# Optimization experiments

Hardware: AMD Instinct MI355X
Metric: run time of the kernel (lower is better)

The kernel has to match this reference:

```python
import jax, jax.numpy as jnp
import numpy as np

B, C, H_IMG, W_IMG = 16, 384, 56, 56
NUM_HEADS = 6
HEAD_DIM = C // NUM_HEADS
BN_EPS = 1e-5


def _bn(x, gamma, beta, mean, var):
    # x: [b, ch, n] or [b, ch, h, w]; per-channel affine normalization (eval-mode BatchNorm)
    shape = (1, -1) + (1,) * (x.ndim - 2)
    scale = (gamma / jnp.sqrt(var + BN_EPS)).reshape(shape)
    shift = (beta - mean * gamma / jnp.sqrt(var + BN_EPS)).reshape(shape)
    return x * scale + shift


def setup_inputs() -> dict:
    key = jax.random.key(0)
    ks = jax.random.split(key, 12)
    c2 = 2 * C
    return {
        "x": jax.random.normal(ks[0], (B, C, H_IMG, W_IMG), jnp.float32),
        "qk_w": jax.random.normal(ks[1], (c2, C // 2), jnp.float32) * 0.05,
        "qk_gamma": jax.random.uniform(ks[2], (c2,), jnp.float32, 0.5, 1.5),
        "qk_beta": jax.random.normal(ks[3], (c2,), jnp.float32) * 0.1,
        "qk_mean": jax.random.normal(ks[4], (c2,), jnp.float32) * 0.1,
        "qk_var": jax.random.uniform(ks[5], (c2,), jnp.float32, 0.5, 1.5),
        "pe_w": jax.random.normal(ks[6], (C, 1, 3, 3), jnp.float32) * 0.1,
        "pe_gamma": jax.random.uniform(ks[7], (C,), jnp.float32, 0.5, 1.5),
        "pe_beta": jax.random.normal(ks[8], (C,), jnp.float32) * 0.1,
        "pe_mean": jax.random.normal(ks[9], (C,), jnp.float32) * 0.1,
        "pe_var": jax.random.uniform(ks[10], (C,), jnp.float32, 0.5, 1.5),
    }


def reference(x, qk_w, qk_gamma, qk_beta, qk_mean, qk_var,
              pe_w, pe_gamma, pe_beta, pe_mean, pe_var):
    b, c, h, w = x.shape
    n = h * w
    s = n ** (-0.5)
    nh, hd = NUM_HEADS, HEAD_DIM

    # grouped (groups=2) 1x1 conv: out channels [0:c] from input [0:c/2], [c:2c] from [c/2:c]
    xg = x.reshape(b, 2, c // 2, n)                       # [b, 2, c/2, n]
    wg = qk_w.reshape(2, c, c // 2)                       # [group, out_per_group, in_per_group]
    qk = jnp.einsum('bgin,goi->bgon', xg, wg).reshape(b, 2 * c, n)
    qk = _bn(qk, qk_gamma, qk_beta, qk_mean, qk_var)
    qk = jax.nn.elu(qk) + 1.0

    qk = qk.reshape(b, 2, nh, hd, n)
    q, k = qk[:, 0], qk[:, 1]                             # [b, H, d, n]
    v = x.reshape(b, nh, hd, n)                           # [b, H, d, n]

    # kv = (k*s) @ (v^T * s): [b, H, d, d]
    kv = jnp.einsum('bhdn,bhen->bhde', k * s, v * s)
    # numerator: q^T @ kv -> [b, H, n, d]
    num = jnp.einsum('bhdn,bhde->bhne', q, kv)
    # denominator: q^T @ mean_n(k) -> [b, H, n]
    den = jnp.einsum('bhdn,bhd->bhn', q, k.mean(axis=-1)) + 1e-6
    attn = (num / den[..., None]).transpose(0, 1, 3, 2).reshape(b, c, h, w)

    # depthwise 3x3 conv positional encoding on v (= x) + BN
    pe = jax.lax.conv_general_dilated(
        x, pe_w, window_strides=(1, 1), padding=((1, 1), (1, 1)),
        feature_group_count=c, dimension_numbers=('NCHW', 'OIHW', 'NCHW'))
    pe = _bn(pe, pe_gamma, pe_beta, pe_mean, pe_var)

    return attn + pe
```

## Files before the change

kernel.cpp:

```cpp
#include <hip/hip_runtime.h>
#include <math.h>

#define N_SP 3136
#define BN_EPS 1e-5f

typedef __attribute__((ext_vector_type(8))) short short8;
typedef __attribute__((ext_vector_type(4))) float f32x4;

#define K_SZ    (16*384*N_SP)
#define KVP_OFF (K_SZ)
#define KVP_SZ  (16*6*7*64*80)
#define KVT_OFF (KVP_OFF + KVP_SZ)
#define KVT_FSZ (2*96*80*64/2)
#define WH_OFF  (KVT_OFF + KVT_FSZ)
#define WSPLIT_N (2*384*192)
#define WF_G    (384*192)
#define PWS_OFF (WH_OFF + WSPLIT_N)
#define PSH_OFF (PWS_OFF + 384*9)
#define QSC_OFF (PSH_OFF + 384)
#define QSH_OFF (QSC_OFF + 384)

#define FSWZ(n) ((((n) >> 1) ^ ((n) >> 2)) & 7)

__device__ __forceinline__ void bsplit(float f, ushort& h, ushort& l) {
    uint u = __float_as_uint(f);
    uint hr = (u + 0x7FFFu + ((u >> 16) & 1u)) >> 16;
    h = (ushort)hr;
    float fh = __uint_as_float(hr << 16);
    float fl = f - fh;
    uint v = __float_as_uint(fl);
    l = (ushort)((v + 0x7FFFu + ((v >> 16) & 1u)) >> 16);
}

__global__ __launch_bounds__(256) void p0_prep(
    const float* __restrict__ qk_w, const float* __restrict__ pe_w,
    const float* __restrict__ qk_gamma, const float* __restrict__ qk_beta,
    const float* __restrict__ qk_mean, const float* __restrict__ qk_var,
    const float* __restrict__ pgamma, const float* __restrict__ pbeta,
    const float* __restrict__ pmean, const float* __restrict__ pvar,
    ushort* __restrict__ wfh, ushort* __restrict__ wfl,
    float* __restrict__ pwsc, float* __restrict__ psh,
    float* __restrict__ qsc, float* __restrict__ qsh)
{
    int idx = blockIdx.x * 256 + threadIdx.x;
    if (idx < WSPLIT_N) {
        int g = (idx >= WF_G) ? 1 : 0;
        int rem = idx - g * WF_G;
        int row = rem / 192, k = rem % 192;
        ushort h, l;
        bsplit(qk_w[idx], h, l);
        int dst = g * WF_G + ((row >> 4) * 24 + (k >> 3)) * 128 + (row & 15) * 8 + (k & 7);
        wfh[dst] = h;
        wfl[dst] = l;
    }
    if (idx < 384) {
        float sc = pgamma[idx] / sqrtf(pvar[idx] + BN_EPS);
        psh[idx] = pbeta[idx] - pmean[idx] * sc;
        #pragma unroll
        for (int q = 0; q < 9; ++q) pwsc[idx * 9 + q] = pe_w[idx * 9 + q] * sc;
        float qs = qk_gamma[idx] / sqrtf(qk_var[idx] + BN_EPS);
        qsc[idx] = qs;
        qsh[idx] = qk_beta[idx] - qk_mean[idx] * qs;
    }
}

__global__ __launch_bounds__(256, 4) void k1_k_mfma(
    const float* __restrict__ x, const ushort* __restrict__ wfh, const ushort* __restrict__ wfl,
    const float* __restrict__ gamma, const float* __restrict__ beta,
    const float* __restrict__ mean, const float* __restrict__ var,
    uint* __restrict__ kq)
{
    __shared__ __align__(16) ushort Bh[4096];
    __shared__ __align__(16) ushort Bl[4096];
    __shared__ float scs[192], shs[192];

    const int bx = blockIdx.x;
    const int by = blockIdx.y;
    const int b = blockIdx.z;
    const int t = threadIdx.x;
    const int lane = t & 63, wv = t >> 6;
    const int lg = lane >> 4, l15 = lane & 15;

    f32x4 acc[3][4];
    #pragma unroll
    for (int mf = 0; mf < 3; ++mf)
        #pragma unroll
        for (int nf = 0; nf < 4; ++nf)
            acc[mf][nf] = (f32x4){0.f, 0.f, 0.f, 0.f};

    const float* xg = x + (size_t)(b * 384 + 192) * N_SP + bx * 64;
    const ushort* wfbh = wfh + WF_G;
    const ushort* wfbl = wfl + WF_G;

    for (int i = t; i < 192; i += 256) {
        int ch = 384 + by * 192 + i;
        float sc = gamma[ch] / sqrtf(var[ch] + BN_EPS);
        scs[i] = sc;
        shs[i] = beta[ch] - mean[ch] * sc;
    }

    for (int kt = 0; kt < 3; ++kt) {
        #pragma unroll
        for (int li = 0; li < 2; ++li) {
            int idx = li * 256 + t;
            int kp = idx >> 4;
            int nq = idx & 15;
            int k0 = kp * 2;
            const float* px = xg + (size_t)(kt * 64 + k0) * N_SP + nq * 4;
            float4 v0 = *(const float4*)px;
            float4 v1 = *(const float4*)(px + N_SP);
            ushort h0[4], l0[4], h1[4], l1[4];
            float a0[4] = {v0.x, v0.y, v0.z, v0.w};
            float a1[4] = {v1.x, v1.y, v1.z, v1.w};
            #pragma unroll
            for (int i2 = 0; i2 < 4; ++i2) { bsplit(a0[i2], h0[i2], l0[i2]); bsplit(a1[i2], h1[i2], l1[i2]); }
            int kb = k0 >> 3, ks = kp & 3;
            #pragma unroll
            for (int i2 = 0; i2 < 4; ++i2) {
                int n = nq * 4 + i2;
                int chunk = n * 8 + (kb ^ FSWZ(n));
                ((uint*)Bh)[chunk * 4 + ks] = (uint)h0[i2] | ((uint)h1[i2] << 16);
                ((uint*)Bl)[chunk * 4 + ks] = (uint)l0[i2] | ((uint)l1[i2] << 16);
            }
        }
        __syncthreads();
        #pragma unroll
        for (int s = 0; s < 2; ++s) {
            int kbq = s * 4 + lg;
            int kglob = kt * 8 + kbq;
            short8 bh[4], bl[4];
            #pragma unroll
            for (int nf = 0; nf < 4; ++nf) {
                int n = nf * 16 + l15;
                int chunk = n * 8 + (kbq ^ FSWZ(n));
                bh[nf] = *(const short8*)&Bh[chunk * 8];
                bl[nf] = *(const short8*)&Bl[chunk * 8];
            }
            #pragma unroll
            for (int mf = 0; mf < 3; ++mf) {
                int rb = by * 12 + wv * 3 + mf;
                int off = (rb * 24 + kglob) * 128 + l15 * 8;
                short8 ah = *(const short8*)&wfbh[off];
                short8 al = *(const short8*)&wfbl[off];
                #pragma unroll
                for (int nf = 0; nf < 4; ++nf) {
                    acc[mf][nf] = __builtin_amdgcn_mfma_f32_16x16x32_bf16(ah, bh[nf], acc[mf][nf], 0, 0, 0);
                    acc[mf][nf] = __builtin_amdgcn_mfma_f32_16x16x32_bf16(ah, bl[nf], acc[mf][nf], 0, 0, 0);
                    acc[mf][nf] = __builtin_amdgcn_mfma_f32_16x16x32_bf16(al, bh[nf], acc[mf][nf], 0, 0, 0);
                }
            }
        }
        __syncthreads();
    }

    size_t obase = ((size_t)b * 384 + by * 192) * N_SP + bx * 64;
    #pragma unroll
    for (int mf = 0; mf < 3; ++mf)
        #pragma unroll
        for (int nf = 0; nf < 4; ++nf) {
            #pragma unroll
            for (int r = 0; r < 4; ++r) {
                int lrow = wv * 48 + mf * 16 + lg * 4 + r;
                float v = acc[mf][nf][r] * scs[lrow] + shs[lrow];
                v = v > 0.f ? v + 1.f : __expf(v);
                ushort hh, ll;
                bsplit(v, hh, ll);
                kq[obase + (size_t)lrow * N_SP + nf * 16 + l15] = (uint)hh | ((uint)ll << 16);
            }
        }
}

__global__ __launch_bounds__(256) void k2_kv_mfma(
    const float* __restrict__ x, const uint* __restrict__ kq,
    float* __restrict__ kv_part)
{
    __shared__ __align__(16) ushort Kh[4096], Kl[4096];
    __shared__ __align__(16) ushort Vh[5120], Vl[5120];

    const int chunk = blockIdx.x;
    const int h = blockIdx.y, b = blockIdx.z;
    const int t = threadIdx.x;
    const int lane = t & 63, wv = t >> 6;
    const int lg = lane >> 4, l15 = lane & 15;

    const uint* kp  = kq + (size_t)(b*384 + h*64) * N_SP;
    const float* vp = x  + (size_t)(b*384 + h*64) * N_SP;

    #pragma unroll
    for (int li = 0; li < 4; ++li) {
        int idx = li * 256 + t;
        int row = 64 + (idx >> 6), col = idx & 63;
        int off = (row * 8 + ((col >> 3) ^ (row & 7))) * 8 + (col & 7);
        Vh[off] = (row == 64) ? (ushort)0x3F80 : (ushort)0;
        Vl[off] = 0;
    }

    f32x4 acc[5];
    #pragma unroll
    for (int nf = 0; nf < 5; ++nf) acc[nf] = (f32x4){0.f, 0.f, 0.f, 0.f};

    for (int sub = 0; sub < 7; ++sub) {
        int n0 = chunk * 448 + sub * 64;
        #pragma unroll
        for (int li = 0; li < 4; ++li) {
            int idx = li * 256 + t;
            int row = idx >> 4, sc = idx & 15;
            int off = (row * 8 + ((sc >> 1) ^ (row & 7))) * 8 + (sc & 1) * 4;
            uint4 kf = *(const uint4*)&kp[(size_t)row * N_SP + n0 + sc * 4];
            ((uint*)&Kh[off])[0] = (kf.x & 0xFFFFu) | (kf.y << 16);
            ((uint*)&Kh[off])[1] = (kf.z & 0xFFFFu) | (kf.w << 16);
            ((uint*)&Kl[off])[0] = (kf.x >> 16) | (kf.y & 0xFFFF0000u);
            ((uint*)&Kl[off])[1] = (kf.z >> 16) | (kf.w & 0xFFFF0000u);
            float4 vf = *(const float4*)&vp[(size_t)row * N_SP + n0 + sc * 4];
            ushort h0,h1,h2,h3,l0,l1,l2,l3;
            bsplit(vf.x,h0,l0); bsplit(vf.y,h1,l1); bsplit(vf.z,h2,l2); bsplit(vf.w,h3,l3);
            ((uint*)&Vh[off])[0] = (uint)h0 | ((uint)h1 << 16);
            ((uint*)&Vh[off])[1] = (uint)h2 | ((uint)h3 << 16);
            ((uint*)&Vl[off])[0] = (uint)l0 | ((uint)l1 << 16);
            ((uint*)&Vl[off])[1] = (uint)l2 | ((uint)l3 << 16);
        }
        __syncthreads();
        #pragma unroll
        for (int s = 0; s < 2; ++s) {
            int arow = wv * 16 + l15;
            int akb = (s * 4 + lg) ^ (arow & 7);
            short8 ah = *(const short8*)&Kh[(arow * 8 + akb) * 8];
            short8 al = *(const short8*)&Kl[(arow * 8 + akb) * 8];
            #pragma unroll
            for (int nf = 0; nf < 5; ++nf) {
                int brow = nf * 16 + l15;
                int bkb = (s * 4 + lg) ^ (brow & 7);
                short8 bh = *(const short8*)&Vh[(brow * 8 + bkb) * 8];
                short8 bl = *(const short8*)&Vl[(brow * 8 + bkb) * 8];
                acc[nf] = __builtin_amdgcn_mfma_f32_16x16x32_bf16(ah, bh, acc[nf], 0, 0, 0);
                acc[nf] = __builtin_amdgcn_mfma_f32_16x16x32_bf16(ah, bl, acc[nf], 0, 0, 0);
                acc[nf] = __builtin_amdgcn_mfma_f32_16x16x32_bf16(al, bh, acc[nf], 0, 0, 0);
            }
        }
        __syncthreads();
    }

    size_t base = (size_t)((b*6 + h)*7 + chunk) * 64 * 80;
    #pragma unroll
    for (int nf = 0; nf < 5; ++nf)
        #pragma unroll
        for (int r = 0; r < 4; ++r) {
            int d = wv * 16 + lg * 4 + r;
            kv_part[base + (size_t)d * 80 + nf * 16 + l15] = acc[nf][r];
        }
}

__global__ __launch_bounds__(256) void k2b_reduce(
    const float* __restrict__ kv_part,
    ushort* __restrict__ kvt_h, ushort* __restrict__ kvt_l)
{
    const int bh = blockIdx.x;
    const int t = threadIdx.x;
    const float inv_n = 1.0f / (float)N_SP;
    const float* base = kv_part + (size_t)bh * 7 * 5120;
    ushort* oh = kvt_h + (size_t)bh * 5120;
    ushort* ol = kvt_l + (size_t)bh * 5120;
    float s[20];
    #pragma unroll
    for (int j = 0; j < 20; ++j) s[j] = 0.f;
    for (int c = 0; c < 7; ++c) {
        #pragma unroll
        for (int j = 0; j < 20; ++j) s[j] += base[c * 5120 + j * 256 + t];
    }
    #pragma unroll
    for (int j = 0; j < 20; ++j) {
        int i = j * 256 + t;
        int d = i / 80, e = i % 80;
        ushort h, l;
        bsplit(s[j] * inv_n, h, l);
        oh[e * 64 + d] = h;
        ol[e * 64 + d] = l;
    }
}

#define ATT_STRIDE 68
__global__ __launch_bounds__(256, 4) void k3_attn_pe(
    const float* __restrict__ x,
    const ushort* __restrict__ wfh, const ushort* __restrict__ wfl,
    const float* __restrict__ qsc, const float* __restrict__ qsh,
    const ushort* __restrict__ kvt_h, const ushort* __restrict__ kvt_l,
    const float* __restrict__ pwsc, const float* __restrict__ psh,
    float* __restrict__ out)
{
    __shared__ __align__(16) float SBF[ATT_STRIDE * 64 + 64];
    ushort* Bh = (ushort*)&SBF[0];
    ushort* Bl = Bh + 4096;

    const int bx = blockIdx.x;
    const int h = blockIdx.y, b = blockIdx.z;
    const int t = threadIdx.x;
    const int lane = t & 63, wv = t >> 6;
    const int lg = lane >> 4, l15 = lane & 15;
    const int n0 = bx * 64;

    const float* xg = x + (size_t)b * 384 * N_SP + n0;

    f32x4 qacc[4];
    #pragma unroll
    for (int nf = 0; nf < 4; ++nf) qacc[nf] = (f32x4){0.f, 0.f, 0.f, 0.f};

    for (int kt = 0; kt < 3; ++kt) {
        #pragma unroll
        for (int li = 0; li < 2; ++li) {
            int idx = li * 256 + t;
            int kp = idx >> 4;
            int nq = idx & 15;
            int k0 = kp * 2;
            const float* px = xg + (size_t)(kt * 64 + k0) * N_SP + nq * 4;
            float4 v0 = *(const float4*)px;
            float4 v1 = *(const float4*)(px + N_SP);
            ushort h0[4], l0[4], h1[4], l1[4];
            float a0[4] = {v0.x, v0.y, v0.z, v0.w};
            float a1[4] = {v1.x, v1.y, v1.z, v1.w};
            #pragma unroll
            for (int i = 0; i < 4; ++i) { bsplit(a0[i], h0[i], l0[i]); bsplit(a1[i], h1[i], l1[i]); }
            int kb = k0 >> 3, ks = kp & 3;
            #pragma unroll
            for (int i = 0; i < 4; ++i) {
                int n = nq * 4 + i;
                int chunk = n * 8 + (kb ^ FSWZ(n));
                ((uint*)Bh)[chunk * 4 + ks] = (uint)h0[i] | ((uint)h1[i] << 16);
                ((uint*)Bl)[chunk * 4 + ks] = (uint)l0[i] | ((uint)l1[i] << 16);
            }
        }
        __syncthreads();
        #pragma unroll
        for (int s = 0; s < 2; ++s) {
            int kbq = s * 4 + lg;
            int kglob = kt * 8 + kbq;
            short8 bh[4], bl[4];
            #pragma unroll
            for (int nf = 0; nf < 4; ++nf) {
                int n = nf * 16 + l15;
                int chunk = n * 8 + (kbq ^ FSWZ(n));
                bh[nf] = *(const short8*)&Bh[chunk * 8];
                bl[nf] = *(const short8*)&Bl[chunk * 8];
            }
            int rb = h * 4 + wv;
            int off = (rb * 24 + kglob) * 128 + l15 * 8;
            short8 ah = *(const short8*)&wfh[off];
            short8 al = *(const short8*)&wfl[off];
            #pragma unroll
            for (int nf = 0; nf < 4; ++nf) {
                qacc[nf] = __builtin_amdgcn_mfma_f32_16x16x32_bf16(ah, bh[nf], qacc[nf], 0, 0, 0);
                qacc[nf] = __builtin_amdgcn_mfma_f32_16x16x32_bf16(ah, bl[nf], qacc[nf], 0, 0, 0);
                qacc[nf] = __builtin_amdgcn_mfma_f32_16x16x32_bf16(al, bh[nf], qacc[nf], 0, 0, 0);
            }
        }
        __syncthreads();
    }

    {
        float sc4[4], sh4[4];
        #pragma unroll
        for (int r = 0; r < 4; ++r) {
            int ch = h * 64 + wv * 16 + lg * 4 + r;
            sc4[r] = qsc[ch];
            sh4[r] = qsh[ch];
        }
        int hc = wv * 4 + lg;
        #pragma unroll
        for (int nf = 0; nf < 4; ++nf) {
            ushort hh[4], ll[4];
            #pragma unroll
            for (int r = 0; r < 4; ++r) {
                float v = qacc[nf][r] * sc4[r] + sh4[r];
                v = v > 0.f ? v + 1.f : __expf(v);
                bsplit(v, hh[r], ll[r]);
            }
            int n = nf * 16 + l15;
            uint2 uh, ul;
            uh.x = (uint)hh[0] | ((uint)hh[1] << 16);
            uh.y = (uint)hh[2] | ((uint)hh[3] << 16);
            ul.x = (uint)ll[0] | ((uint)ll[1] << 16);
            ul.y = (uint)ll[2] | ((uint)ll[3] << 16);
            *(uint2*)(Bh + hc * 256 + n * 4) = uh;
            *(uint2*)(Bl + hc * 256 + n * 4) = ul;
        }
    }
    __syncthreads();

    short8 bqh[2], bql[2];
    #pragma unroll
    for (int s = 0; s < 2; ++s) {
        int hc = (s * 4 + lg) * 2;
        const ushort* ph = Bh + hc * 256 + (wv * 16 + l15) * 4;
        uint2 a0 = *(const uint2*)ph;
        uint2 a1 = *(const uint2*)(ph + 256);
        uint* pp = (uint*)&bqh[s];
        pp[0] = a0.x; pp[1] = a0.y; pp[2] = a1.x; pp[3] = a1.y;
        const ushort* pl = Bl + hc * 256 + (wv * 16 + l15) * 4;
        uint2 c0 = *(const uint2*)pl;
        uint2 c1 = *(const uint2*)(pl + 256);
        uint* qq = (uint*)&bql[s];
        qq[0] = c0.x; qq[1] = c0.y; qq[2] = c1.x; qq[3] = c1.y;
    }
    __syncthreads();

    const ushort* ahb = kvt_h + (size_t)(b * 6 + h) * 5120;
    const ushort* alb = kvt_l + (size_t)(b * 6 + h) * 5120;
    f32x4 pacc[5];
    #pragma unroll
    for (int m = 0; m < 5; ++m) pacc[m] = (f32x4){0.f, 0.f, 0.f, 0.f};
    #pragma unroll
    for (int s = 0; s < 2; ++s) {
        #pragma unroll
        for (int m = 0; m < 5; ++m) {
            int off = (m * 16 + l15) * 64 + (s * 4 + lg) * 8;
            short8 ah = *(const short8*)&ahb[off];
            short8 al = *(const short8*)&alb[off];
            pacc[m] = __builtin_amdgcn_mfma_f32_16x16x32_bf16(ah, bqh[s], pacc[m], 0, 0, 0);
            pacc[m] = __builtin_amdgcn_mfma_f32_16x16x32_bf16(ah, bql[s], pacc[m], 0, 0, 0);
            pacc[m] = __builtin_amdgcn_mfma_f32_16x16x32_bf16(al, bqh[s], pacc[m], 0, 0, 0);
        }
    }
    {
        int ncol = wv * 16 + l15;
        #pragma unroll
        for (int m = 0; m < 4; ++m)
            #pragma unroll
            for (int r = 0; r < 4; ++r)
                SBF[(m * 16 + lg * 4 + r) * ATT_STRIDE + ncol] = pacc[m][r];
        if (lg == 0)
            SBF[ATT_STRIDE * 64 + ncol] = pacc[4][0];
    }
    __syncthreads();

    const int tx = t & 15, ty = t >> 4;
    const int p0 = n0 + tx * 4;
    const int y = p0 / 56, xc = p0 % 56;
    float den[4];
    #pragma unroll
    for (int p = 0; p < 4; ++p) den[p] = SBF[ATT_STRIDE * 64 + tx * 4 + p] + 1e-6f;
    #pragma unroll
    for (int j = 0; j < 4; ++j) {
        int c = h * 64 + ty * 4 + j;
        const float* xp = x + ((size_t)b * 384 + c) * N_SP;
        float s6[3][6];
        #pragma unroll
        for (int dy = 0; dy < 3; ++dy) {
            int yy = y + dy - 1;
            bool yok = (yy >= 0) && (yy < 56);
            float4 mid = make_float4(0.f, 0.f, 0.f, 0.f);
            float lf = 0.f, rt = 0.f;
            if (yok) {
                const float* xr = xp + yy * 56;
                mid = *(const float4*)&xr[xc];
                if (xc > 0)  lf = xr[xc - 1];
                if (xc < 52) rt = xr[xc + 4];
            }
            s6[dy][0] = lf;  s6[dy][1] = mid.x; s6[dy][2] = mid.y;
            s6[dy][3] = mid.z; s6[dy][4] = mid.w; s6[dy][5] = rt;
        }
        float w9[9];
        #pragma unroll
        for (int q = 0; q < 9; ++q) w9[q] = pwsc[c * 9 + q];
        float sh2 = psh[c];
        float4 r;
        float* pr = (float*)&r;
        #pragma unroll
        for (int p = 0; p < 4; ++p) {
            float conv = 0.f;
            #pragma unroll
            for (int dy = 0; dy < 3; ++dy)
                #pragma unroll
                for (int dx = 0; dx < 3; ++dx)
                    conv += w9[dy * 3 + dx] * s6[dy][p + dx];
            pr[p] = SBF[(ty * 4 + j) * ATT_STRIDE + tx * 4 + p] / den[p] + conv + sh2;
        }
        *(float4*)&out[((size_t)b * 384 + c) * N_SP + p0] = r;
    }
}

extern "C" void kernel_launch(void* const* d_in, const int* in_sizes, int n_in,
                              void* d_out, int out_size, void* d_ws, size_t ws_size,
                              hipStream_t stream)
{
    const float* x        = (const float*)d_in[0];
    const float* qk_w     = (const float*)d_in[1];
    const float* qk_gamma = (const float*)d_in[2];
    const float* qk_beta  = (const float*)d_in[3];
    const float* qk_mean  = (const float*)d_in[4];
    const float* qk_var   = (const float*)d_in[5];
    const float* pe_w     = (const float*)d_in[6];
    const float* pe_gamma = (const float*)d_in[7];
    const float* pe_beta  = (const float*)d_in[8];
    const float* pe_mean  = (const float*)d_in[9];
    const float* pe_var   = (const float*)d_in[10];
    float* out = (float*)d_out;

    float* ws      = (float*)d_ws;
    uint* kq       = (uint*)ws;
    float* kv_part = ws + KVP_OFF;
    ushort* kvt_h  = (ushort*)(ws + KVT_OFF);
    ushort* kvt_l  = kvt_h + 96 * 5120;
    ushort* wfh    = (ushort*)(ws + WH_OFF);
    ushort* wfl    = wfh + WSPLIT_N;
    float* pwsc    = ws + PWS_OFF;
    float* psh     = ws + PSH_OFF;
    float* qsc     = ws + QSC_OFF;
    float* qsh     = ws + QSH_OFF;

    hipLaunchKernelGGL(p0_prep, dim3((WSPLIT_N + 255)/256), dim3(256), 0, stream,
                       qk_w, pe_w, qk_gamma, qk_beta, qk_mean, qk_var,
                       pe_gamma, pe_beta, pe_mean, pe_var,
                       wfh, wfl, pwsc, psh, qsc, qsh);
    dim3 g1(49, 2, 16);
    hipLaunchKernelGGL(k1_k_mfma, g1, dim3(256), 0, stream,
                       x, wfh, wfl, qk_gamma, qk_beta, qk_mean, qk_var, kq);
    dim3 g2(7, 6, 16);
    hipLaunchKernelGGL(k2_kv_mfma, g2, dim3(256), 0, stream, x, kq, kv_part);
    hipLaunchKernelGGL(k2b_reduce, dim3(96), dim3(256), 0, stream,
                       kv_part, kvt_h, kvt_l);
    dim3 g3(49, 6, 16);
    hipLaunchKernelGGL(k3_attn_pe, g3, dim3(256), 0, stream,
                       x, wfh, wfl, qsc, qsh, kvt_h, kvt_l, pwsc, psh, out);
}
```

Before: 209.7 us.

## Compute three heads per block in attention kernel to reuse staged x tile

Each k3 block now handles three heads of one group instead of one head, so the bf16-split x tile loaded into shared memory for the Q projection is reused across three heads' MFMA accumulations. The grid shrinks from 6 to 2 in the head dimension. This cuts redundant global loads and split conversions of x by a factor of three. In exchange it needs 48 accumulator vectors per thread, which raises register pressure and may lower occupancy, and there are fewer blocks to fill the device.

```diff
diff --git a/kernel.cpp b/kernel.cpp
--- a/kernel.cpp
+++ b/kernel.cpp
@@ -292,7 +292,8 @@
     ushort* Bl = Bh + 4096;
 
     const int bx = blockIdx.x;
-    const int h = blockIdx.y, b = blockIdx.z;
+    const int hgrp = blockIdx.y;
+    const int b = blockIdx.z;
     const int t = threadIdx.x;
     const int lane = t & 63, wv = t >> 6;
     const int lg = lane >> 4, l15 = lane & 15;
@@ -300,9 +301,11 @@
 
     const float* xg = x + (size_t)b * 384 * N_SP + n0;
 
-    f32x4 qacc[4];
-    #pragma unroll
-    for (int nf = 0; nf < 4; ++nf) qacc[nf] = (f32x4){0.f, 0.f, 0.f, 0.f};
+    f32x4 qacc[3][4];
+    #pragma unroll
+    for (int hh = 0; hh < 3; ++hh)
+        #pragma unroll
+        for (int nf = 0; nf < 4; ++nf) qacc[hh][nf] = (f32x4){0.f, 0.f, 0.f, 0.f};
 
     for (int kt = 0; kt < 3; ++kt) {
         #pragma unroll
@@ -341,139 +344,149 @@
                 bh[nf] = *(const short8*)&Bh[chunk * 8];
                 bl[nf] = *(const short8*)&Bl[chunk * 8];
             }
-            int rb = h * 4 + wv;
-            int off = (rb * 24 + kglob) * 128 + l15 * 8;
-            short8 ah = *(const short8*)&wfh[off];
-            short8 al = *(const short8*)&wfl[off];
-            #pragma unroll
-            for (int nf = 0; nf < 4; ++nf) {
-                qacc[nf] = __builtin_amdgcn_mfma_f32_16x16x32_bf16(ah, bh[nf], qacc[nf], 0, 0, 0);
-                qacc[nf] = __builtin_amdgcn_mfma_f32_16x16x32_bf16(ah, bl[nf], qacc[nf], 0, 0, 0);
-                qacc[nf] = __builtin_amdgcn_mfma_f32_16x16x32_bf16(al, bh[nf], qacc[nf], 0, 0, 0);
-            }
-        }
-        __syncthreads();
-    }
-
-    {
-        float sc4[4], sh4[4];
-        #pragma unroll
-        for (int r = 0; r < 4; ++r) {
-            int ch = h * 64 + wv * 16 + lg * 4 + r;
-            sc4[r] = qsc[ch];
-            sh4[r] = qsh[ch];
-        }
-        int hc = wv * 4 + lg;
-        #pragma unroll
-        for (int nf = 0; nf < 4; ++nf) {
-            ushort hh[4], ll[4];
-            #pragma unroll
-            for (int r = 0; r < 4; ++r) {
-                float v = qacc[nf][r] * sc4[r] + sh4[r];
-                v = v > 0.f ? v + 1.f : __expf(v);
-                bsplit(v, hh[r], ll[r]);
-            }
-            int n = nf * 16 + l15;
-            uint2 uh, ul;
-            uh.x = (uint)hh[0] | ((uint)hh[1] << 16);
-            uh.y = (uint)hh[2] | ((uint)hh[3] << 16);
-            ul.x = (uint)ll[0] | ((uint)ll[1] << 16);
-            ul.y = (uint)ll[2] | ((uint)ll[3] << 16);
-            *(uint2*)(Bh + hc * 256 + n * 4) = uh;
-            *(uint2*)(Bl + hc * 256 + n * 4) = ul;
-        }
-    }
-    __syncthreads();
-
-    short8 bqh[2], bql[2];
-    #pragma unroll
-    for (int s = 0; s < 2; ++s) {
-        int hc = (s * 4 + lg) * 2;
-        const ushort* ph = Bh + hc * 256 + (wv * 16 + l15) * 4;
-        uint2 a0 = *(const uint2*)ph;
-        uint2 a1 = *(const uint2*)(ph + 256);
-        uint* pp = (uint*)&bqh[s];
-        pp[0] = a0.x; pp[1] = a0.y; pp[2] = a1.x; pp[3] = a1.y;
-        const ushort* pl = Bl + hc * 256 + (wv * 16 + l15) * 4;
-        uint2 c0 = *(const uint2*)pl;
-        uint2 c1 = *(const uint2*)(pl + 256);
-        uint* qq = (uint*)&bql[s];
-        qq[0] = c0.x; qq[1] = c0.y; qq[2] = c1.x; qq[3] = c1.y;
-    }
-    __syncthreads();
-
-    const ushort* ahb = kvt_h + (size_t)(b * 6 + h) * 5120;
-    const ushort* alb = kvt_l + (size_t)(b * 6 + h) * 5120;
-    f32x4 pacc[5];
-    #pragma unroll
-    for (int m = 0; m < 5; ++m) pacc[m] = (f32x4){0.f, 0.f, 0.f, 0.f};
-    #pragma unroll
-    for (int s = 0; s < 2; ++s) {
-        #pragma unroll
-        for (int m = 0; m < 5; ++m) {
-            int off = (m * 16 + l15) * 64 + (s * 4 + lg) * 8;
-            short8 ah = *(const short8*)&ahb[off];
-            short8 al = *(const short8*)&alb[off];
-            pacc[m] = __builtin_amdgcn_mfma_f32_16x16x32_bf16(ah, bqh[s], pacc[m], 0, 0, 0);
-            pacc[m] = __builtin_amdgcn_mfma_f32_16x16x32_bf16(ah, bql[s], pacc[m], 0, 0, 0);
-            pacc[m] = __builtin_amdgcn_mfma_f32_16x16x32_bf16(al, bqh[s], pacc[m], 0, 0, 0);
-        }
-    }
-    {
-        int ncol = wv * 16 + l15;
-        #pragma unroll
-        for (int m = 0; m < 4; ++m)
-            #pragma unroll
-            for (int r = 0; r < 4; ++r)
-                SBF[(m * 16 + lg * 4 + r) * ATT_STRIDE + ncol] = pacc[m][r];
-        if (lg == 0)
-            SBF[ATT_STRIDE * 64 + ncol] = pacc[4][0];
-    }
-    __syncthreads();
+            #pragma unroll
+            for (int hh = 0; hh < 3; ++hh) {
+                int rb = (hgrp * 3 + hh) * 4 + wv;
+                int off = (rb * 24 + kglob) * 128 + l15 * 8;
+                short8 ah = *(const short8*)&wfh[off];
+                short8 al = *(const short8*)&wfl[off];
+                #pragma unroll
+                for (int nf = 0; nf < 4; ++nf) {
+                    qacc[hh][nf] = __builtin_amdgcn_mfma_f32_16x16x32_bf16(ah, bh[nf], qacc[hh][nf], 0, 0, 0);
+                    qacc[hh][nf] = __builtin_amdgcn_mfma_f32_16x16x32_bf16(ah, bl[nf], qacc[hh][nf], 0, 0, 0);
+                    qacc[hh][nf] = __builtin_amdgcn_mfma_f32_16x16x32_bf16(al, bh[nf], qacc[hh][nf], 0, 0, 0);
+                }
+            }
+        }
+        __syncthreads();
+    }
 
     const int tx = t & 15, ty = t >> 4;
     const int p0 = n0 + tx * 4;
     const int y = p0 / 56, xc = p0 % 56;
-    float den[4];
-    #pragma unroll
-    for (int p = 0; p < 4; ++p) den[p] = SBF[ATT_STRIDE * 64 + tx * 4 + p] + 1e-6f;
-    #pragma unroll
-    for (int j = 0; j < 4; ++j) {
-        int c = h * 64 + ty * 4 + j;
-        const float* xp = x + ((size_t)b * 384 + c) * N_SP;
-        float s6[3][6];
-        #pragma unroll
-        for (int dy = 0; dy < 3; ++dy) {
-            int yy = y + dy - 1;
-            bool yok = (yy >= 0) && (yy < 56);
-            float4 mid = make_float4(0.f, 0.f, 0.f, 0.f);
-            float lf = 0.f, rt = 0.f;
-            if (yok) {
-                const float* xr = xp + yy * 56;
-                mid = *(const float4*)&xr[xc];
-                if (xc > 0)  lf = xr[xc - 1];
-                if (xc < 52) rt = xr[xc + 4];
-            }
-            s6[dy][0] = lf;  s6[dy][1] = mid.x; s6[dy][2] = mid.y;
-            s6[dy][3] = mid.z; s6[dy][4] = mid.w; s6[dy][5] = rt;
-        }
-        float w9[9];
-        #pragma unroll
-        for (int q = 0; q < 9; ++q) w9[q] = pwsc[c * 9 + q];
-        float sh2 = psh[c];
-        float4 r;
-        float* pr = (float*)&r;
-        #pragma unroll
-        for (int p = 0; p < 4; ++p) {
-            float conv = 0.f;
-            #pragma unroll
-            for (int dy = 0; dy < 3; ++dy)
+
+    #pragma unroll 1
+    for (int hh = 0; hh < 3; ++hh) {
+        const int h = hgrp * 3 + hh;
+
+        {
+            float sc4[4], sh4[4];
+            #pragma unroll
+            for (int r = 0; r < 4; ++r) {
+                int ch = h * 64 + wv * 16 + lg * 4 + r;
+                sc4[r] = qsc[ch];
+                sh4[r] = qsh[ch];
+            }
+            int hc = wv * 4 + lg;
+            #pragma unroll
+            for (int nf = 0; nf < 4; ++nf) {
+                ushort hhq[4], llq[4];
                 #pragma unroll
-                for (int dx = 0; dx < 3; ++dx)
-                    conv += w9[dy * 3 + dx] * s6[dy][p + dx];
-            pr[p] = SBF[(ty * 4 + j) * ATT_STRIDE + tx * 4 + p] / den[p] + conv + sh2;
-        }
-        *(float4*)&out[((size_t)b * 384 + c) * N_SP + p0] = r;
+                for (int r = 0; r < 4; ++r) {
+                    float v = qacc[hh][nf][r] * sc4[r] + sh4[r];
+                    v = v > 0.f ? v + 1.f : __expf(v);
+                    bsplit(v, hhq[r], llq[r]);
+                }
+                int n = nf * 16 + l15;
+                uint2 uh, ul;
+                uh.x = (uint)hhq[0] | ((uint)hhq[1] << 16);
+                uh.y = (uint)hhq[2] | ((uint)hhq[3] << 16);
+                ul.x = (uint)llq[0] | ((uint)llq[1] << 16);
+                ul.y = (uint)llq[2] | ((uint)llq[3] << 16);
+                *(uint2*)(Bh + hc * 256 + n * 4) = uh;
+                *(uint2*)(Bl + hc * 256 + n * 4) = ul;
+            }
+        }
+        __syncthreads();
+
+        short8 bqh[2], bql[2];
+        #pragma unroll
+        for (int s = 0; s < 2; ++s) {
+            int hc = (s * 4 + lg) * 2;
+            const ushort* ph = Bh + hc * 256 + (wv * 16 + l15) * 4;
+            uint2 a0 = *(const uint2*)ph;
+            uint2 a1 = *(const uint2*)(ph + 256);
+            uint* pp = (uint*)&bqh[s];
+            pp[0] = a0.x; pp[1] = a0.y; pp[2] = a1.x; pp[3] = a1.y;
+            const ushort* pl = Bl + hc * 256 + (wv * 16 + l15) * 4;
+            uint2 c0 = *(const uint2*)pl;
+            uint2 c1 = *(const uint2*)(pl + 256);
+            uint* qq = (uint*)&bql[s];
+            qq[0] = c0.x; qq[1] = c0.y; qq[2] = c1.x; qq[3] = c1.y;
+        }
+        __syncthreads();
+
+        const ushort* ahb = kvt_h + (size_t)(b * 6 + h) * 5120;
+        const ushort* alb = kvt_l + (size_t)(b * 6 + h) * 5120;
+        f32x4 pacc[5];
+        #pragma unroll
+        for (int m = 0; m < 5; ++m) pacc[m] = (f32x4){0.f, 0.f, 0.f, 0.f};
+        #pragma unroll
+        for (int s = 0; s < 2; ++s) {
+            #pragma unroll
+            for (int m = 0; m < 5; ++m) {
+                int off = (m * 16 + l15) * 64 + (s * 4 + lg) * 8;
+                short8 ah = *(const short8*)&ahb[off];
+                short8 al = *(const short8*)&alb[off];
+                pacc[m] = __builtin_amdgcn_mfma_f32_16x16x32_bf16(ah, bqh[s], pacc[m], 0, 0, 0);
+                pacc[m] = __builtin_amdgcn_mfma_f32_16x16x32_bf16(ah, bql[s], pacc[m], 0, 0, 0);
+                pacc[m] = __builtin_amdgcn_mfma_f32_16x16x32_bf16(al, bqh[s], pacc[m], 0, 0, 0);
+            }
+        }
+        {
+            int ncol = wv * 16 + l15;
+            #pragma unroll
+            for (int m = 0; m < 4; ++m)
+                #pragma unroll
+                for (int r = 0; r < 4; ++r)
+                    SBF[(m * 16 + lg * 4 + r) * ATT_STRIDE + ncol] = pacc[m][r];
+            if (lg == 0)
+                SBF[ATT_STRIDE * 64 + ncol] = pacc[4][0];
+        }
+        __syncthreads();
+
+        float den4[4];
+        #pragma unroll
+        for (int p = 0; p < 4; ++p) den4[p] = SBF[ATT_STRIDE * 64 + tx * 4 + p] + 1e-6f;
+        #pragma unroll
+        for (int j = 0; j < 4; ++j) {
+            int c = h * 64 + ty * 4 + j;
+            const float* xp = x + ((size_t)b * 384 + c) * N_SP;
+            float s6[3][6];
+            #pragma unroll
+            for (int dy = 0; dy < 3; ++dy) {
+                int yy = y + dy - 1;
+                bool yok = (yy >= 0) && (yy < 56);
+                float4 mid = make_float4(0.f, 0.f, 0.f, 0.f);
+                float lf = 0.f, rt = 0.f;
+                if (yok) {
+                    const float* xr = xp + yy * 56;
+                    mid = *(const float4*)&xr[xc];
+                    if (xc > 0)  lf = xr[xc - 1];
+                    if (xc < 52) rt = xr[xc + 4];
+                }
+                s6[dy][0] = lf;  s6[dy][1] = mid.x; s6[dy][2] = mid.y;
+                s6[dy][3] = mid.z; s6[dy][4] = mid.w; s6[dy][5] = rt;
+            }
+            float w9[9];
+            #pragma unroll
+            for (int q = 0; q < 9; ++q) w9[q] = pwsc[c * 9 + q];
+            float sh2 = psh[c];
+            float4 r;
+            float* pr = (float*)&r;
+            #pragma unroll
+            for (int p = 0; p < 4; ++p) {
+                float conv = 0.f;
+                #pragma unroll
+                for (int dy = 0; dy < 3; ++dy)
+                    #pragma unroll
+                    for (int dx = 0; dx < 3; ++dx)
+                        conv += w9[dy * 3 + dx] * s6[dy][p + dx];
+                pr[p] = SBF[(ty * 4 + j) * ATT_STRIDE + tx * 4 + p] / den4[p] + conv + sh2;
+            }
+            *(float4*)&out[((size_t)b * 384 + c) * N_SP + p0] = r;
+        }
+        __syncthreads();
     }
 }
 
@@ -517,7 +530,7 @@
     hipLaunchKernelGGL(k2_kv_mfma, g2, dim3(256), 0, stream, x, kq, kv_part);
     hipLaunchKernelGGL(k2b_reduce, dim3(96), dim3(256), 0, stream,
                        kv_part, kvt_h, kvt_l);
-    dim3 g3(49, 6, 16);
+    dim3 g3(49, 2, 16);
     hipLaunchKernelGGL(k3_attn_pe, g3, dim3(256), 0, stream,
                        x, wfh, wfl, qsc, qsh, kvt_h, kvt_l, pwsc, psh, out);
 }
```

New measurement: 266.7 us. +27.2%, slower.
